# Optimization experiments

Measured on AMD Instinct MI355X. Metric: run time of the kernel, lower is better.

Reference implementation:

```python
import jax, jax.numpy as jnp
import numpy as np

N_NODES = 100000
N_EDGES = 1600000
IN_DIM = 256
OUT_DIM = 128
NEG_SLOPE = 0.2
LAMBDA = 0.5  # fixed (non-learnable), clamped to [0,1] in original
EPS = 1e-8


def setup_inputs() -> dict:
    key = jax.random.key(0)
    ks = jax.random.split(key, 8)
    x = jax.random.normal(ks[0], (N_NODES, IN_DIM), dtype=jnp.float32)
    edge_index = jax.random.randint(ks[1], (2, N_EDGES), 0, N_NODES, dtype=jnp.int64)
    beta = jax.random.uniform(ks[2], (N_EDGES,), dtype=jnp.float32)
    # Learned parameters (xavier-scale random instead of the zero init so the
    # attention path is exercised numerically).
    s_gat = (6.0 / (IN_DIM + OUT_DIM)) ** 0.5
    W_gat = jax.random.uniform(ks[3], (OUT_DIM, IN_DIM), jnp.float32, -s_gat, s_gat)
    att_src = jax.random.normal(ks[4], (OUT_DIM,), dtype=jnp.float32) * 0.1
    att_dst = jax.random.normal(ks[5], (OUT_DIM,), dtype=jnp.float32) * 0.1
    bias = jnp.zeros((OUT_DIM,), dtype=jnp.float32)
    W_fixed = jax.random.uniform(ks[6], (OUT_DIM, IN_DIM), jnp.float32, -s_gat, s_gat)
    return {
        "x": x, "edge_index": edge_index, "beta": beta,
        "W_gat": W_gat, "att_src": att_src, "att_dst": att_dst,
        "bias": bias, "W_fixed": W_fixed,
    }


def reference(x, edge_index, beta, W_gat, att_src, att_dst, bias, W_fixed):
    N = x.shape[0]
    src, dst = edge_index[0], edge_index[1]

    # ---- STAGATE attention branch (hL) ----
    h = x @ W_gat.T                       # (N, D)
    h_src = h[src]                        # (E, D) gather
    h_dst = h[dst]                        # (E, D) gather
    e = h_src @ att_src + h_dst @ att_dst # (E,)
    e = jnp.where(e >= 0, e, NEG_SLOPE * e)   # LeakyReLU
    alpha = jax.nn.sigmoid(e)
    denom = jax.ops.segment_sum(alpha, dst, num_segments=N) + EPS  # (N,)
    alpha = alpha / denom[dst]
    hL = jax.ops.segment_sum(h_src * alpha[:, None], dst, num_segments=N)
    hL = hL + bias

    # ---- fixed-beta branch (hF) ----
    xW = x @ W_fixed.T                    # (N, D)
    hF = jax.ops.segment_sum(xW[src] * beta[:, None], dst, num_segments=N)

    # ---- fuse + activation ----
    lam = jnp.clip(jnp.float32(LAMBDA), 0.0, 1.0)
    out = lam * hL + (1.0 - lam) * hF
    return jax.nn.elu(out)
```

## Files before the change

### kernel.cpp

```cpp
#include <hip/hip_runtime.h>
#include <math.h>

#define N_NODES 100000
#define N_EDGES 1600000
#define IN_DIM 256
#define OUT_DIM 128
#define NEG_SLOPE 0.2f
#define LAMBDA 0.5f
#define EPS 1e-8f

#define FIX_SCALE 67108864.0f
#define FIX_INV   (1.0f / 67108864.0f)
#define CNT_SHIFT 46

#define OFF_HB    ((size_t)0)
#define OFF_XB    ((size_t)6400000)
#define OFF_WC    ((size_t)12800000)
#define OFF_ASRC  ((size_t)12832768)
#define OFF_ADST  ((size_t)12932768)
#define OFF_PACK  ((size_t)13032768)
#define OFF_COUNT ((size_t)13232768)
#define OFF_OFFS  ((size_t)13332768)
#define OFF_BSUM  ((size_t)13432768)
#define OFF_TMP   ((size_t)13433792)
#define OFF_REC   ((size_t)19833792)
#define WS_FLOATS ((size_t)26233792)

#define SCAN_BLOCKS ((N_NODES + 255) / 256)

typedef __attribute__((ext_vector_type(8))) short bf16x8;
typedef __attribute__((ext_vector_type(4))) float f32x4;

__device__ __forceinline__ unsigned short f2b(float f) {
    unsigned u = __float_as_uint(f);
    u += 0x7FFFu + ((u >> 16) & 1u);
    return (unsigned short)(u >> 16);
}
__device__ __forceinline__ float b2f_lo(unsigned u) { return __uint_as_float(u << 16); }
__device__ __forceinline__ float b2f_hi(unsigned u) { return __uint_as_float(u & 0xFFFF0000u); }

__global__ __launch_bounds__(256) void convert_w(
    const float* __restrict__ Wg, const float* __restrict__ Wf,
    ushort* __restrict__ Wc)
{
    int g = blockIdx.x * 256 + threadIdx.x;
    int e4  = g * 4;
    int row = e4 >> 8;
    int col = e4 & 255;
    const float* src = (row < 128) ? (Wg + (size_t)row * 256 + col)
                                   : (Wf + (size_t)(row - 128) * 256 + col);
    float4 v = *(const float4*)src;
    ushort4 p;
    p.x = f2b(v.x); p.y = f2b(v.y); p.z = f2b(v.z); p.w = f2b(v.w);
    *(ushort4*)(Wc + (size_t)row * 256 + col) = p;
}

__global__ __launch_bounds__(256) void gemm_mfma(
    const float* __restrict__ x, const ushort* __restrict__ Wc,
    ushort* __restrict__ hb, ushort* __restrict__ xb)
{
    __shared__ ushort As[64 * 264];
    __shared__ ushort Bs[4 * 256 * 8];
    const int tid  = threadIdx.x;
    const int wv   = tid >> 6;
    const int lane = tid & 63;
    const int quad = lane >> 4;
    const int l16  = lane & 15;
    const int nb   = blockIdx.x * 64;

    f32x4 acc[4][4];
#pragma unroll
    for (int mt = 0; mt < 4; ++mt)
#pragma unroll
        for (int nt = 0; nt < 4; ++nt) acc[mt][nt] = (f32x4){0.f, 0.f, 0.f, 0.f};

#pragma unroll
    for (int it = 0; it < 16; ++it) {
        int f   = tid + it * 256;
        int row = f >> 6;
        int c4  = (f & 63) << 2;
        int gn  = nb + row; if (gn >= N_NODES) gn = N_NODES - 1;
        float4 v = *(const float4*)(x + (size_t)gn * IN_DIM + c4);
        ushort4 p;
        p.x = f2b(v.x); p.y = f2b(v.y); p.z = f2b(v.z); p.w = f2b(v.w);
        *(ushort4*)(&As[row * 264 + c4]) = p;
    }

    for (int kc = 0; kc < 256; kc += 32) {
        __syncthreads();
        {
            const int n = tid;
#pragma unroll
            for (int b = 0; b < 4; ++b) {
                bf16x8 w = *(const bf16x8*)(Wc + (size_t)n * 256 + kc + b * 8);
                *(bf16x8*)(&Bs[((size_t)b * 256 + n) * 8]) = w;
            }
        }
        __syncthreads();

        bf16x8 afr[4], bfr[4];
#pragma unroll
        for (int mt = 0; mt < 4; ++mt)
            afr[mt] = *(const bf16x8*)(&As[(mt * 16 + l16) * 264 + kc + quad * 8]);
#pragma unroll
        for (int nt = 0; nt < 4; ++nt) {
            int n = wv * 64 + nt * 16 + l16;
            bfr[nt] = *(const bf16x8*)(&Bs[((size_t)quad * 256 + n) * 8]);
        }
#pragma unroll
        for (int mt = 0; mt < 4; ++mt)
#pragma unroll
            for (int nt = 0; nt < 4; ++nt)
                acc[mt][nt] = __builtin_amdgcn_mfma_f32_16x16x32_bf16(
                    afr[mt], bfr[nt], acc[mt][nt], 0, 0, 0);
    }

    ushort* outp = (wv < 2) ? hb : xb;
    const int ncol0 = (wv & 1) * 64;
#pragma unroll
    for (int mt = 0; mt < 4; ++mt) {
#pragma unroll
        for (int nt = 0; nt < 4; ++nt) {
            int coln = ncol0 + nt * 16 + l16;
#pragma unroll
            for (int r = 0; r < 4; ++r) {
                int node = nb + mt * 16 + quad * 4 + r;
                if (node < N_NODES)
                    outp[(size_t)node * 128 + coln] = f2b(acc[mt][nt][r]);
            }
        }
    }
}

__global__ __launch_bounds__(256) void node_scalars(
    const ushort* __restrict__ hb, const float* __restrict__ att_s,
    const float* __restrict__ att_d, float* __restrict__ a_src,
    float* __restrict__ a_dst)
{
    int node = blockIdx.x * 8 + (threadIdx.x >> 5);
    int l    = threadIdx.x & 31;
    if (node >= N_NODES) return;
    uint2 u = *(const uint2*)(hb + (size_t)node * 128 + l * 4);
    float f0 = b2f_lo(u.x), f1 = b2f_hi(u.x), f2 = b2f_lo(u.y), f3 = b2f_hi(u.y);
    float4 s = *(const float4*)(att_s + l * 4);
    float4 d = *(const float4*)(att_d + l * 4);
    float ss = f0 * s.x + f1 * s.y + f2 * s.z + f3 * s.w;
    float dd = f0 * d.x + f1 * d.y + f2 * d.z + f3 * d.w;
#pragma unroll
    for (int m = 1; m < 32; m <<= 1) {
        ss += __shfl_xor(ss, m);
        dd += __shfl_xor(dd, m);
    }
    if (l == 0) { a_src[node] = ss; a_dst[node] = dd; }
}

__global__ __launch_bounds__(256) void edge_prep(
    const int* __restrict__ ei, const float* __restrict__ a_src,
    const float* __restrict__ a_dst, unsigned long long* __restrict__ pack,
    int4* __restrict__ tmp)
{
    int e = blockIdx.x * 256 + threadIdx.x;
    int s = ei[e];
    int d = ei[N_EDGES + e];
    s = s < 0 ? 0 : (s >= N_NODES ? N_NODES - 1 : s);
    d = d < 0 ? 0 : (d >= N_NODES ? N_NODES - 1 : d);
    float ev = a_src[s] + a_dst[d];
    ev = ev >= 0.f ? ev : NEG_SLOPE * ev;
    float al = 1.f / (1.f + expf(-ev));
    unsigned fix = (unsigned)(al * FIX_SCALE + 0.5f);
    unsigned long long old = atomicAdd(pack + d,
        ((unsigned long long)1 << CNT_SHIFT) | (unsigned long long)fix);
    int pos = (int)(old >> CNT_SHIFT);
    tmp[e] = make_int4(s, d, pos, __float_as_int(al));
}

__global__ __launch_bounds__(256) void scan1(
    const unsigned long long* __restrict__ pack, int* __restrict__ count,
    int* __restrict__ offs, int* __restrict__ bsum)
{
    __shared__ int s[256];
    int i = blockIdx.x * 256 + threadIdx.x;
    int v = (i < N_NODES) ? (int)(pack[i] >> CNT_SHIFT) : 0;
    if (i < N_NODES) count[i] = v;
    s[threadIdx.x] = v;
    __syncthreads();
    for (int off = 1; off < 256; off <<= 1) {
        int t = (threadIdx.x >= off) ? s[threadIdx.x - off] : 0;
        __syncthreads();
        s[threadIdx.x] += t;
        __syncthreads();
    }
    if (i < N_NODES) offs[i] = s[threadIdx.x] - v;
    if (threadIdx.x == 255) bsum[blockIdx.x] = s[255];
}

__global__ __launch_bounds__(512) void scan2(int* __restrict__ bsum)
{
    __shared__ int s[512];
    int v = (threadIdx.x < SCAN_BLOCKS) ? bsum[threadIdx.x] : 0;
    s[threadIdx.x] = v;
    __syncthreads();
    for (int off = 1; off < 512; off <<= 1) {
        int t = (threadIdx.x >= off) ? s[threadIdx.x - off] : 0;
        __syncthreads();
        s[threadIdx.x] += t;
        __syncthreads();
    }
    if (threadIdx.x < SCAN_BLOCKS) bsum[threadIdx.x] = s[threadIdx.x] - v;
}

__global__ __launch_bounds__(256) void scan3(
    int* __restrict__ offs, const int* __restrict__ bsum)
{
    int i = blockIdx.x * 256 + threadIdx.x;
    if (i < N_NODES) offs[i] += bsum[blockIdx.x];
}

__global__ __launch_bounds__(256) void scatter_rec(
    const int4* __restrict__ tmp, const unsigned long long* __restrict__ pack,
    const int* __restrict__ offs, const float* __restrict__ beta,
    float4* __restrict__ rec)
{
    int e = blockIdx.x * 256 + threadIdx.x;
    int4 t = tmp[e];
    float al = __int_as_float(t.w);
    unsigned long long p = pack[t.y];
    float denom = (float)(p & (((unsigned long long)1 << CNT_SHIFT) - 1)) * FIX_INV;
    float c1 = LAMBDA * al / (denom + EPS);
    float c2 = (1.f - LAMBDA) * beta[e];
    int slot = offs[t.y] + t.z;
    rec[slot] = make_float4(__int_as_float(t.x), c1, c2, 0.f);
}

__global__ __launch_bounds__(256) void segment_reduce(
    const ushort* __restrict__ hb, const ushort* __restrict__ xb,
    const float4* __restrict__ rec, const int* __restrict__ offs,
    const int* __restrict__ count, const float* __restrict__ bias,
    float* __restrict__ out)
{
    int wave = (blockIdx.x * 256 + threadIdx.x) >> 6;
    int lane = threadIdx.x & 63;
    if (wave >= N_NODES) return;
    int start = offs[wave];
    int cnt   = count[wave];
    const bool hhalf = lane < 32;
    const ushort* base = hhalf ? hb : xb;
    const int l4 = (lane & 31) * 4;

    float4 acc = make_float4(0.f, 0.f, 0.f, 0.f);
    int k = 0;
    for (; k + 2 <= cnt; k += 2) {
        float4 r0 = rec[start + k];
        float4 r1 = rec[start + k + 1];
        int   s0 = __float_as_int(r0.x);
        int   s1 = __float_as_int(r1.x);
        float c0 = hhalf ? r0.y : r0.z;
        float c1 = hhalf ? r1.y : r1.z;
        uint2 u0 = *(const uint2*)(base + (size_t)s0 * 128 + l4);
        uint2 u1 = *(const uint2*)(base + (size_t)s1 * 128 + l4);
        acc.x += c0 * b2f_lo(u0.x); acc.y += c0 * b2f_hi(u0.x);
        acc.z += c0 * b2f_lo(u0.y); acc.w += c0 * b2f_hi(u0.y);
        acc.x += c1 * b2f_lo(u1.x); acc.y += c1 * b2f_hi(u1.x);
        acc.z += c1 * b2f_lo(u1.y); acc.w += c1 * b2f_hi(u1.y);
    }
    if (k < cnt) {
        float4 r0 = rec[start + k];
        int   s0 = __float_as_int(r0.x);
        float c0 = hhalf ? r0.y : r0.z;
        uint2 u0 = *(const uint2*)(base + (size_t)s0 * 128 + l4);
        acc.x += c0 * b2f_lo(u0.x); acc.y += c0 * b2f_hi(u0.x);
        acc.z += c0 * b2f_lo(u0.y); acc.w += c0 * b2f_hi(u0.y);
    }

    acc.x += __shfl_xor(acc.x, 32);
    acc.y += __shfl_xor(acc.y, 32);
    acc.z += __shfl_xor(acc.z, 32);
    acc.w += __shfl_xor(acc.w, 32);

    if (hhalf) {
        float4 b = *(const float4*)(bias + l4);
        float4 o;
        o.x = acc.x + LAMBDA * b.x;
        o.y = acc.y + LAMBDA * b.y;
        o.z = acc.z + LAMBDA * b.z;
        o.w = acc.w + LAMBDA * b.w;
        o.x = o.x > 0.f ? o.x : expm1f(o.x);
        o.y = o.y > 0.f ? o.y : expm1f(o.y);
        o.z = o.z > 0.f ? o.z : expm1f(o.z);
        o.w = o.w > 0.f ? o.w : expm1f(o.w);
        *(float4*)(out + (size_t)wave * OUT_DIM + l4) = o;
    }
}

extern "C" void kernel_launch(void* const* d_in, const int* in_sizes, int n_in,
                              void* d_out, int out_size, void* d_ws, size_t ws_size,
                              hipStream_t stream)
{
    const float* x     = (const float*)d_in[0];
    const int*   ei    = (const int*)d_in[1];
    const float* beta  = (const float*)d_in[2];
    const float* Wg    = (const float*)d_in[3];
    const float* att_s = (const float*)d_in[4];
    const float* att_d = (const float*)d_in[5];
    const float* bias  = (const float*)d_in[6];
    const float* Wf    = (const float*)d_in[7];
    float* out = (float*)d_out;
    float* ws  = (float*)d_ws;

    if (ws_size < WS_FLOATS * sizeof(float)) return;

    ushort* hb   = (ushort*)(ws + OFF_HB);
    ushort* xb   = (ushort*)(ws + OFF_XB);
    ushort* Wc   = (ushort*)(ws + OFF_WC);
    float*  asrc = ws + OFF_ASRC;
    float*  adst = ws + OFF_ADST;
    unsigned long long* pack = (unsigned long long*)(ws + OFF_PACK);
    int*    count = (int*)(ws + OFF_COUNT);
    int*    offs  = (int*)(ws + OFF_OFFS);
    int*    bsum  = (int*)(ws + OFF_BSUM);
    int4*   tmp   = (int4*)(ws + OFF_TMP);
    float4* rec   = (float4*)(ws + OFF_REC);

    hipMemsetAsync(pack, 0, (size_t)N_NODES * sizeof(unsigned long long), stream);

    convert_w<<<64, 256, 0, stream>>>(Wg, Wf, Wc);
    gemm_mfma<<<(N_NODES + 63) / 64, 256, 0, stream>>>(x, Wc, hb, xb);
    node_scalars<<<(N_NODES + 7) / 8, 256, 0, stream>>>(hb, att_s, att_d, asrc, adst);
    edge_prep<<<N_EDGES / 256, 256, 0, stream>>>(ei, asrc, adst, pack, tmp);
    scan1<<<SCAN_BLOCKS, 256, 0, stream>>>(pack, count, offs, bsum);
    scan2<<<1, 512, 0, stream>>>(bsum);
    scan3<<<SCAN_BLOCKS, 256, 0, stream>>>(offs, bsum);
    scatter_rec<<<N_EDGES / 256, 256, 0, stream>>>(tmp, pack, offs, beta, rec);
    segment_reduce<<<(N_NODES * 64 + 255) / 256, 256, 0, stream>>>(hb, xb, rec, offs, count, bias, out);
}
```

Baseline: 488.0 us.

## Fuse node scalars into GEMM epilogue, pre-tile weights, widen segment-reduce loads

```diff
diff --git a/kernel.cpp b/kernel.cpp
--- a/kernel.cpp
+++ b/kernel.cpp
@@ -39,25 +39,28 @@
 __device__ __forceinline__ float b2f_lo(unsigned u) { return __uint_as_float(u << 16); }
 __device__ __forceinline__ float b2f_hi(unsigned u) { return __uint_as_float(u & 0xFFFF0000u); }
 
-__global__ __launch_bounds__(256) void convert_w(
+__global__ __launch_bounds__(256) void convert_w2(
     const float* __restrict__ Wg, const float* __restrict__ Wf,
-    ushort* __restrict__ Wc)
-{
-    int g = blockIdx.x * 256 + threadIdx.x;
-    int e4  = g * 4;
-    int row = e4 >> 8;
-    int col = e4 & 255;
-    const float* src = (row < 128) ? (Wg + (size_t)row * 256 + col)
-                                   : (Wf + (size_t)(row - 128) * 256 + col);
-    float4 v = *(const float4*)src;
-    ushort4 p;
-    p.x = f2b(v.x); p.y = f2b(v.y); p.z = f2b(v.z); p.w = f2b(v.w);
-    *(ushort4*)(Wc + (size_t)row * 256 + col) = p;
+    ushort* __restrict__ Wc2)
+{
+    int g  = blockIdx.x * 256 + threadIdx.x;
+    int n  = g & 255;
+    int kb = g >> 8;
+    const float* src = (n < 128) ? (Wg + (size_t)n * 256 + kb * 8)
+                                 : (Wf + (size_t)(n - 128) * 256 + kb * 8);
+    float4 a = *(const float4*)(src);
+    float4 b = *(const float4*)(src + 4);
+    ushort p[8];
+    p[0] = f2b(a.x); p[1] = f2b(a.y); p[2] = f2b(a.z); p[3] = f2b(a.w);
+    p[4] = f2b(b.x); p[5] = f2b(b.y); p[6] = f2b(b.z); p[7] = f2b(b.w);
+    *(bf16x8*)(Wc2 + (size_t)g * 8) = *(bf16x8*)p;
 }
 
 __global__ __launch_bounds__(256) void gemm_mfma(
-    const float* __restrict__ x, const ushort* __restrict__ Wc,
-    ushort* __restrict__ hb, ushort* __restrict__ xb)
+    const float* __restrict__ x, const ushort* __restrict__ Wc2,
+    const float* __restrict__ att_s, const float* __restrict__ att_d,
+    ushort* __restrict__ hb, ushort* __restrict__ xb,
+    float* __restrict__ a_src, float* __restrict__ a_dst)
 {
     __shared__ ushort As[64 * 264];
     __shared__ ushort Bs[4 * 256 * 8];
@@ -88,13 +91,10 @@
 
     for (int kc = 0; kc < 256; kc += 32) {
         __syncthreads();
-        {
-            const int n = tid;
-#pragma unroll
-            for (int b = 0; b < 4; ++b) {
-                bf16x8 w = *(const bf16x8*)(Wc + (size_t)n * 256 + kc + b * 8);
-                *(bf16x8*)(&Bs[((size_t)b * 256 + n) * 8]) = w;
-            }
+#pragma unroll
+        for (int it = 0; it < 4; ++it) {
+            int off = (it * 256 + tid) * 8;
+            *(bf16x8*)(&Bs[off]) = *(const bf16x8*)(Wc2 + (size_t)kc * 256 + off);
         }
         __syncthreads();
 
@@ -104,7 +104,7 @@
             afr[mt] = *(const bf16x8*)(&As[(mt * 16 + l16) * 264 + kc + quad * 8]);
 #pragma unroll
         for (int nt = 0; nt < 4; ++nt) {
-            int n = wv * 64 + nt * 16 + l16;
+            int n = (wv & 1) * 64 + ((wv >> 1) << 7) + nt * 16 + l16;
             bfr[nt] = *(const bf16x8*)(&Bs[((size_t)quad * 256 + n) * 8]);
         }
 #pragma unroll
@@ -115,43 +115,58 @@
                     afr[mt], bfr[nt], acc[mt][nt], 0, 0, 0);
     }
 
-    ushort* outp = (wv < 2) ? hb : xb;
-    const int ncol0 = (wv & 1) * 64;
-#pragma unroll
-    for (int mt = 0; mt < 4; ++mt) {
-#pragma unroll
-        for (int nt = 0; nt < 4; ++nt) {
-            int coln = ncol0 + nt * 16 + l16;
-#pragma unroll
-            for (int r = 0; r < 4; ++r) {
-                int node = nb + mt * 16 + quad * 4 + r;
-                if (node < N_NODES)
-                    outp[(size_t)node * 128 + coln] = f2b(acc[mt][nt][r]);
+    __syncthreads();
+    {
+        const int colbase = (wv >> 1) * 128 + (wv & 1) * 64;
+#pragma unroll
+        for (int mt = 0; mt < 4; ++mt)
+#pragma unroll
+            for (int nt = 0; nt < 4; ++nt) {
+                int col = colbase + nt * 16 + l16;
+#pragma unroll
+                for (int r = 0; r < 4; ++r)
+                    As[(mt * 16 + quad * 4 + r) * 264 + col] = f2b(acc[mt][nt][r]);
             }
+    }
+    __syncthreads();
+
+    {
+        const int row = tid >> 2;
+        const int q   = tid & 3;
+        const int gn  = nb + row;
+        bf16x8 v[8];
+#pragma unroll
+        for (int j = 0; j < 8; ++j)
+            v[j] = *(const bf16x8*)(&As[row * 264 + q * 64 + j * 8]);
+        if (gn < N_NODES) {
+            ushort* dst = (q < 2) ? (hb + (size_t)gn * 128 + q * 64)
+                                  : (xb + (size_t)gn * 128 + (q - 2) * 64);
+#pragma unroll
+            for (int j = 0; j < 8; ++j)
+                *(bf16x8*)(dst + j * 8) = v[j];
         }
-    }
-}
-
-__global__ __launch_bounds__(256) void node_scalars(
-    const ushort* __restrict__ hb, const float* __restrict__ att_s,
-    const float* __restrict__ att_d, float* __restrict__ a_src,
-    float* __restrict__ a_dst)
-{
-    int node = blockIdx.x * 8 + (threadIdx.x >> 5);
-    int l    = threadIdx.x & 31;
-    if (node >= N_NODES) return;
-    uint2 u = *(const uint2*)(hb + (size_t)node * 128 + l * 4);
-    float f0 = b2f_lo(u.x), f1 = b2f_hi(u.x), f2 = b2f_lo(u.y), f3 = b2f_hi(u.y);
-    float4 s = *(const float4*)(att_s + l * 4);
-    float4 d = *(const float4*)(att_d + l * 4);
-    float ss = f0 * s.x + f1 * s.y + f2 * s.z + f3 * s.w;
-    float dd = f0 * d.x + f1 * d.y + f2 * d.z + f3 * d.w;
-#pragma unroll
-    for (int m = 1; m < 32; m <<= 1) {
-        ss += __shfl_xor(ss, m);
-        dd += __shfl_xor(dd, m);
-    }
-    if (l == 0) { a_src[node] = ss; a_dst[node] = dd; }
+        if (q < 2) {
+            const float4* as4 = (const float4*)att_s;
+            const float4* ad4 = (const float4*)att_d;
+            float ss = 0.f, dd = 0.f;
+#pragma unroll
+            for (int j = 0; j < 8; ++j) {
+#pragma unroll
+                for (int hv = 0; hv < 2; ++hv) {
+                    float4 sa = as4[q * 16 + j * 2 + hv];
+                    float4 da = ad4[q * 16 + j * 2 + hv];
+                    unsigned u0 = ((const unsigned*)&v[j])[hv * 2];
+                    unsigned u1 = ((const unsigned*)&v[j])[hv * 2 + 1];
+                    float f0 = b2f_lo(u0), f1 = b2f_hi(u0), f2 = b2f_lo(u1), f3 = b2f_hi(u1);
+                    ss += f0 * sa.x + f1 * sa.y + f2 * sa.z + f3 * sa.w;
+                    dd += f0 * da.x + f1 * da.y + f2 * da.z + f3 * da.w;
+                }
+            }
+            ss += __shfl_xor(ss, 1);
+            dd += __shfl_xor(dd, 1);
+            if (q == 0 && gn < N_NODES) { a_src[gn] = ss; a_dst[gn] = dd; }
+        }
+    }
 }
 
 __global__ __launch_bounds__(256) void edge_prep(
@@ -159,19 +174,24 @@
     const float* __restrict__ a_dst, unsigned long long* __restrict__ pack,
     int4* __restrict__ tmp)
 {
-    int e = blockIdx.x * 256 + threadIdx.x;
-    int s = ei[e];
-    int d = ei[N_EDGES + e];
-    s = s < 0 ? 0 : (s >= N_NODES ? N_NODES - 1 : s);
-    d = d < 0 ? 0 : (d >= N_NODES ? N_NODES - 1 : d);
-    float ev = a_src[s] + a_dst[d];
-    ev = ev >= 0.f ? ev : NEG_SLOPE * ev;
-    float al = 1.f / (1.f + expf(-ev));
-    unsigned fix = (unsigned)(al * FIX_SCALE + 0.5f);
-    unsigned long long old = atomicAdd(pack + d,
-        ((unsigned long long)1 << CNT_SHIFT) | (unsigned long long)fix);
-    int pos = (int)(old >> CNT_SHIFT);
-    tmp[e] = make_int4(s, d, pos, __float_as_int(al));
+    const int bb = blockIdx.x * 1024 + threadIdx.x;
+#pragma unroll
+    for (int k = 0; k < 4; ++k) {
+        int e = bb + k * 256;
+        if (e >= N_EDGES) break;
+        int s = ei[e];
+        int d = ei[N_EDGES + e];
+        s = s < 0 ? 0 : (s >= N_NODES ? N_NODES - 1 : s);
+        d = d < 0 ? 0 : (d >= N_NODES ? N_NODES - 1 : d);
+        float ev = a_src[s] + a_dst[d];
+        ev = ev >= 0.f ? ev : NEG_SLOPE * ev;
+        float al = 1.f / (1.f + __expf(-ev));
+        unsigned fix = (unsigned)(al * FIX_SCALE + 0.5f);
+        unsigned long long old = atomicAdd(pack + d,
+            ((unsigned long long)1 << CNT_SHIFT) | (unsigned long long)fix);
+        int pos = (int)(old >> CNT_SHIFT);
+        tmp[e] = make_int4(s, d, pos, __float_as_int(al));
+    }
 }
 
 __global__ __launch_bounds__(256) void scan1(
@@ -241,54 +261,65 @@
     int wave = (blockIdx.x * 256 + threadIdx.x) >> 6;
     int lane = threadIdx.x & 63;
     if (wave >= N_NODES) return;
-    int start = offs[wave];
-    int cnt   = count[wave];
-    const bool hhalf = lane < 32;
-    const ushort* base = hhalf ? hb : xb;
-    const int l4 = (lane & 31) * 4;
-
-    float4 acc = make_float4(0.f, 0.f, 0.f, 0.f);
+    const int start = offs[wave];
+    const int cnt   = count[wave];
+    const int sub  = lane >> 5;
+    const int half = (lane >> 4) & 1;
+    const int li   = lane & 15;
+    const ushort* __restrict__ base = half ? xb : hb;
+
+    float av[8] = {0.f, 0.f, 0.f, 0.f, 0.f, 0.f, 0.f, 0.f};
     int k = 0;
-    for (; k + 2 <= cnt; k += 2) {
-        float4 r0 = rec[start + k];
-        float4 r1 = rec[start + k + 1];
-        int   s0 = __float_as_int(r0.x);
-        int   s1 = __float_as_int(r1.x);
-        float c0 = hhalf ? r0.y : r0.z;
-        float c1 = hhalf ? r1.y : r1.z;
-        uint2 u0 = *(const uint2*)(base + (size_t)s0 * 128 + l4);
-        uint2 u1 = *(const uint2*)(base + (size_t)s1 * 128 + l4);
-        acc.x += c0 * b2f_lo(u0.x); acc.y += c0 * b2f_hi(u0.x);
-        acc.z += c0 * b2f_lo(u0.y); acc.w += c0 * b2f_hi(u0.y);
-        acc.x += c1 * b2f_lo(u1.x); acc.y += c1 * b2f_hi(u1.x);
-        acc.z += c1 * b2f_lo(u1.y); acc.w += c1 * b2f_hi(u1.y);
-    }
-    if (k < cnt) {
-        float4 r0 = rec[start + k];
-        int   s0 = __float_as_int(r0.x);
-        float c0 = hhalf ? r0.y : r0.z;
-        uint2 u0 = *(const uint2*)(base + (size_t)s0 * 128 + l4);
-        acc.x += c0 * b2f_lo(u0.x); acc.y += c0 * b2f_hi(u0.x);
-        acc.z += c0 * b2f_lo(u0.y); acc.w += c0 * b2f_hi(u0.y);
-    }
-
-    acc.x += __shfl_xor(acc.x, 32);
-    acc.y += __shfl_xor(acc.y, 32);
-    acc.z += __shfl_xor(acc.z, 32);
-    acc.w += __shfl_xor(acc.w, 32);
-
-    if (hhalf) {
-        float4 b = *(const float4*)(bias + l4);
-        float4 o;
-        o.x = acc.x + LAMBDA * b.x;
-        o.y = acc.y + LAMBDA * b.y;
-        o.z = acc.z + LAMBDA * b.z;
-        o.w = acc.w + LAMBDA * b.w;
-        o.x = o.x > 0.f ? o.x : expm1f(o.x);
-        o.y = o.y > 0.f ? o.y : expm1f(o.y);
-        o.z = o.z > 0.f ? o.z : expm1f(o.z);
-        o.w = o.w > 0.f ? o.w : expm1f(o.w);
-        *(float4*)(out + (size_t)wave * OUT_DIM + l4) = o;
+    for (; k + 4 <= cnt; k += 4) {
+        float4 rA = rec[start + k + sub];
+        float4 rB = rec[start + k + 2 + sub];
+        int   sA = __float_as_int(rA.x);
+        int   sB = __float_as_int(rB.x);
+        float cA = half ? rA.z : rA.y;
+        float cB = half ? rB.z : rB.y;
+        uint4 uA = *(const uint4*)(base + (size_t)sA * 128 + li * 8);
+        uint4 uB = *(const uint4*)(base + (size_t)sB * 128 + li * 8);
+        av[0] += cA * b2f_lo(uA.x); av[1] += cA * b2f_hi(uA.x);
+        av[2] += cA * b2f_lo(uA.y); av[3] += cA * b2f_hi(uA.y);
+        av[4] += cA * b2f_lo(uA.z); av[5] += cA * b2f_hi(uA.z);
+        av[6] += cA * b2f_lo(uA.w); av[7] += cA * b2f_hi(uA.w);
+        av[0] += cB * b2f_lo(uB.x); av[1] += cB * b2f_hi(uB.x);
+        av[2] += cB * b2f_lo(uB.y); av[3] += cB * b2f_hi(uB.y);
+        av[4] += cB * b2f_lo(uB.z); av[5] += cB * b2f_hi(uB.z);
+        av[6] += cB * b2f_lo(uB.w); av[7] += cB * b2f_hi(uB.w);
+    }
+    for (; k < cnt; k += 2) {
+        int kk  = k + sub;
+        int idx = start + (kk < cnt ? kk : cnt - 1);
+        float4 r = rec[idx];
+        int   s = __float_as_int(r.x);
+        float c = half ? r.z : r.y;
+        c = (kk < cnt) ? c : 0.f;
+        uint4 u = *(const uint4*)(base + (size_t)s * 128 + li * 8);
+        av[0] += c * b2f_lo(u.x); av[1] += c * b2f_hi(u.x);
+        av[2] += c * b2f_lo(u.y); av[3] += c * b2f_hi(u.y);
+        av[4] += c * b2f_lo(u.z); av[5] += c * b2f_hi(u.z);
+        av[6] += c * b2f_lo(u.w); av[7] += c * b2f_hi(u.w);
+    }
+
+#pragma unroll
+    for (int j = 0; j < 8; ++j) av[j] += __shfl_xor(av[j], 32);
+#pragma unroll
+    for (int j = 0; j < 8; ++j) av[j] += __shfl_xor(av[j], 16);
+
+    if (lane < 16) {
+        const float4* b4 = (const float4*)(bias + li * 8);
+        float4 b0 = b4[0], b1 = b4[1];
+        float o[8];
+        o[0] = av[0] + LAMBDA * b0.x; o[1] = av[1] + LAMBDA * b0.y;
+        o[2] = av[2] + LAMBDA * b0.z; o[3] = av[3] + LAMBDA * b0.w;
+        o[4] = av[4] + LAMBDA * b1.x; o[5] = av[5] + LAMBDA * b1.y;
+        o[6] = av[6] + LAMBDA * b1.z; o[7] = av[7] + LAMBDA * b1.w;
+#pragma unroll
+        for (int j = 0; j < 8; ++j) o[j] = o[j] > 0.f ? o[j] : expm1f(o[j]);
+        float* op = out + (size_t)wave * OUT_DIM + li * 8;
+        *(float4*)(op)     = make_float4(o[0], o[1], o[2], o[3]);
+        *(float4*)(op + 4) = make_float4(o[4], o[5], o[6], o[7]);
     }
 }
 
@@ -311,7 +342,7 @@
 
     ushort* hb   = (ushort*)(ws + OFF_HB);
     ushort* xb   = (ushort*)(ws + OFF_XB);
-    ushort* Wc   = (ushort*)(ws + OFF_WC);
+    ushort* Wc2  = (ushort*)(ws + OFF_WC);
     float*  asrc = ws + OFF_ASRC;
     float*  adst = ws + OFF_ADST;
     unsigned long long* pack = (unsigned long long*)(ws + OFF_PACK);
@@ -323,10 +354,9 @@
 
     hipMemsetAsync(pack, 0, (size_t)N_NODES * sizeof(unsigned long long), stream);
 
-    convert_w<<<64, 256, 0, stream>>>(Wg, Wf, Wc);
-    gemm_mfma<<<(N_NODES + 63) / 64, 256, 0, stream>>>(x, Wc, hb, xb);
-    node_scalars<<<(N_NODES + 7) / 8, 256, 0, stream>>>(hb, att_s, att_d, asrc, adst);
-    edge_prep<<<N_EDGES / 256, 256, 0, stream>>>(ei, asrc, adst, pack, tmp);
+    convert_w2<<<32, 256, 0, stream>>>(Wg, Wf, Wc2);
+    gemm_mfma<<<(N_NODES + 63) / 64, 256, 0, stream>>>(x, Wc2, att_s, att_d, hb, xb, asrc, adst);
+    edge_prep<<<(N_EDGES + 1023) / 1024, 256, 0, stream>>>(ei, asrc, adst, pack, tmp);
     scan1<<<SCAN_BLOCKS, 256, 0, stream>>>(pack, count, offs, bsum);
     scan2<<<1, 512, 0, stream>>>(bsum);
     scan3<<<SCAN_BLOCKS, 256, 0, stream>>>(offs, bsum);
```

Result: no change. 482.9 us (-1.0%).
